# Performance work log

Hardware: AMD Instinct MI355X
Metric: run time of the kernel (lower is better)

The kernel has to match this reference:

```python
import jax, jax.numpy as jnp
import numpy as np

NUM_CLASSES = 10  # matches label fill_max; original iterates over train_label.unique()


def setup_inputs() -> dict:
    key = jax.random.key(0)
    k1, k2, k3 = jax.random.split(key, 3)
    n, m, d = 8192, 50000, 128
    x = jax.random.normal(k1, (n, d), dtype=jnp.float32)
    train_pts = jax.random.normal(k2, (m, d), dtype=jnp.float32)
    train_label = jax.random.randint(k3, (m,), 0, NUM_CLASSES, dtype=jnp.int32)
    return {"x": x, "train_pts": train_pts, "train_label": train_label, "k": 10}


def reference(x, train_pts, train_label, k):
    # Euclidean distance matrix [n, m]; same math as expand/pow/sum without the
    x2 = jnp.sum(x * x, axis=1, keepdims=True)          # [n, 1]
    y2 = jnp.sum(train_pts * train_pts, axis=1)         # [m]
    sq = x2 + y2[None, :] - 2.0 * (x @ train_pts.T)     # [n, m]
    dist = jnp.sqrt(jnp.maximum(sq, 0.0))
    # k smallest distances -> neighbor indices
    _, idx = jax.lax.top_k(-dist, k)                    # [n, k]
    votes = train_label[idx]                            # [n, k]
    # per-class vote counts; original loop: for lab in sorted unique labels,
    # who = count >= best -> ties go to the LARGEST label
    counts = jnp.sum(jax.nn.one_hot(votes, NUM_CLASSES, dtype=jnp.int32), axis=1)  # [n, C]
    winner = (NUM_CLASSES - 1) - jnp.argmax(counts[:, ::-1], axis=1)
    return winner.astype(train_label.dtype)
```

## Files before the change

kernel.cpp:

```cpp
#include <hip/hip_runtime.h>
#include <float.h>
#include <limits.h>

#define N_Q 8192
#define M_PTS 50000
#define DIM 128
#define KNN 10
#define NCLS 10
#define NCHUNK 16
#define TPC 196
#define CPC 8
#define NCAND (NCHUNK*CPC)
#define NSEL 24
#define TPL 4
#define QPB 64
#define SBIAS 256.0f
#define YTHREADS 200000
#define PTHREADS 232768
#define ATHREADS 232944

typedef __attribute__((ext_vector_type(8))) int i32x8;
typedef __attribute__((ext_vector_type(4))) float f32x4;
typedef unsigned int u32;

__device__ __forceinline__ u32 to_e4m3(float f) {
    u32 u = __float_as_uint(f);
    u32 s = (u >> 24) & 0x80u;
    u32 au = u & 0x7FFFFFFFu;
    if (au > 0x43E00000u) au = 0x43E00000u;
    u32 r = au + 0x0007FFFFu + ((au >> 20) & 1u);
    int e = (int)(r >> 23) - 127;
    if (e < -6) return s;
    return s | (u32)((e + 7) << 3) | ((r >> 20) & 7u);
}

__device__ __forceinline__ u32 pack4_e4m3(float4 v, float sc) {
    return to_e4m3(sc * v.x) | (to_e4m3(sc * v.y) << 8) |
           (to_e4m3(sc * v.z) << 16) | (to_e4m3(sc * v.w) << 24);
}

__global__ __launch_bounds__(256) void prep_kernel(
    const float4* __restrict__ x4, const float4* __restrict__ y4,
    u32* __restrict__ xb8, u32* __restrict__ yt8, float* __restrict__ y2) {
    int t = blockIdx.x * 256 + threadIdx.x;
    if (t < YTHREADS) {
        int T = t >> 6, l = t & 63, nr = l & 15, g = l >> 4;
        const float4* src = y4 + ((size_t)(T * 16 + nr) * DIM + g * 32) / 4;
        u32 w[8];
        float ss = 0.f;
        #pragma unroll
        for (int i = 0; i < 8; ++i) {
            float4 v = src[i];
            ss += v.x * v.x + v.y * v.y + v.z * v.z + v.w * v.w;
            w[i] = pack4_e4m3(v, 1.0f);
        }
        uint4* dst = (uint4*)(yt8 + (size_t)T * 512 + l * 8);
        dst[0] = make_uint4(w[0], w[1], w[2], w[3]);
        dst[1] = make_uint4(w[4], w[5], w[6], w[7]);
        ss += __shfl_xor(ss, 16, 64);
        ss += __shfl_xor(ss, 32, 64);
        if (l < 16) y2[T * 16 + l] = ss;
    } else if (t < PTHREADS) {
        int tx = t - YTHREADS, row = tx >> 2, g = tx & 3;
        const float4* src = x4 + ((size_t)row * DIM + g * 32) / 4;
        u32 w[8];
        #pragma unroll
        for (int i = 0; i < 8; ++i) w[i] = pack4_e4m3(src[i], -2.0f);
        uint4* dst = (uint4*)(xb8 + (size_t)row * 32 + g * 8);
        dst[0] = make_uint4(w[0], w[1], w[2], w[3]);
        dst[1] = make_uint4(w[4], w[5], w[6], w[7]);
    } else if (t < ATHREADS) {
        y2[M_PTS + (t - PTHREADS)] = FLT_MAX;
    }
}

__global__ __launch_bounds__(256, 8) void knn_filter(
    const u32* __restrict__ xb8, const u32* __restrict__ yt8,
    const float* __restrict__ y2, u32* __restrict__ ckey) {
    const int lane = threadIdx.x & 63;
    const int wid  = threadIdx.x >> 6;
    const int g    = lane >> 4;
    const int nrow = lane & 15;
    const int chunk = blockIdx.x;
    const int qb    = blockIdx.y;
    const int qw = qb * QPB + wid * 16;

    i32x8 a = *(const i32x8*)(xb8 + (size_t)(qw + nrow) * 32 + g * 8);

    float ts[4][TPL];
    #pragma unroll
    for (int r = 0; r < 4; ++r)
        #pragma unroll
        for (int l = 0; l < TPL; ++l) ts[r][l] = FLT_MAX;

    const u32* ytp = yt8 + (size_t)chunk * TPC * 512 + lane * 8;
    const float* y2p = y2 + chunk * TPC * 16 + nrow;

    for (int t = 0; t < TPC; ++t) {
        i32x8 b = *(const i32x8*)(ytp + (size_t)t * 512);
        float y2n = y2p[t * 16] + SBIAS;
        f32x4 cq = {y2n, y2n, y2n, y2n};
        f32x4 d = __builtin_amdgcn_mfma_scale_f32_16x16x128_f8f6f4(
            a, b, cq, 0, 0, 0, 0x7F7F7F7F, 0, 0x7F7F7F7F);
        u32 rel = (u32)(t * 16) | (u32)nrow;
        #pragma unroll
        for (int i = 0; i < 4; ++i) {
            float key = __uint_as_float((__float_as_uint(d[i]) & 0xFFFFF000u) | rel);
            float o0 = ts[i][0], o1 = ts[i][1], o2 = ts[i][2];
            ts[i][0] = fminf(o0, key);
            ts[i][1] = __builtin_amdgcn_fmed3f(key, o0, o1);
            ts[i][2] = __builtin_amdgcn_fmed3f(key, o1, o2);
            ts[i][3] = __builtin_amdgcn_fmed3f(key, o2, ts[i][3]);
        }
    }

    __shared__ u32 smem[QPB * 65];
    #pragma unroll
    for (int r = 0; r < 4; ++r) {
        int ql = wid * 16 + g * 4 + r;
        #pragma unroll
        for (int l = 0; l < TPL; ++l)
            smem[ql * 65 + nrow * TPL + l] = __float_as_uint(ts[r][l]);
    }
    __syncthreads();
    if (threadIdx.x < QPB) {
        int ql = threadIdx.x;
        float bs[CPC];
        #pragma unroll
        for (int i = 0; i < CPC; ++i) bs[i] = FLT_MAX;
        for (int e = 0; e < 16 * TPL; ++e) {
            float f = __uint_as_float(smem[ql * 65 + e]);
            #pragma unroll
            for (int q2 = 0; q2 < CPC; ++q2) {
                float mn = fminf(bs[q2], f);
                f = fmaxf(bs[q2], f);
                bs[q2] = mn;
            }
        }
        u32* dst = ckey + ((size_t)(qb * QPB + ql) * NCHUNK + chunk) * CPC;
        #pragma unroll
        for (int i = 0; i < CPC; ++i) dst[i] = __float_as_uint(bs[i]);
    }
}

__global__ __launch_bounds__(256) void knn_finalize(
    const u32* __restrict__ ckey, const float* __restrict__ x,
    const float* __restrict__ y, const int* __restrict__ labels,
    int* __restrict__ out) {
    const int lane = threadIdx.x & 63;
    const int wid  = threadIdx.x >> 6;
    const int qbase = blockIdx.x * 8;
    const int ql = wid * 2 + (lane >> 5);
    const int sl = lane & 31;

    __shared__ u32 skey[8][NCAND];
    __shared__ int sidx[8][NSEL];
    __shared__ double sex[8][NSEL];

    for (int i = threadIdx.x; i < 8 * NCAND; i += 256)
        skey[i >> 7][i & 127] = ckey[(size_t)(qbase + (i >> 7)) * NCAND + (i & 127)];
    __syncthreads();

    {
        u32 ke[4];
        int rank[4];
        #pragma unroll
        for (int r0 = 0; r0 < 4; ++r0) {
            ke[r0] = skey[ql][r0 * 32 + sl];
            rank[r0] = 0;
        }
        for (int j = 0; j < NCAND; ++j) {
            u32 kj = skey[ql][j];
            #pragma unroll
            for (int r0 = 0; r0 < 4; ++r0)
                rank[r0] += (kj < ke[r0] || (kj == ke[r0] && j < r0 * 32 + sl)) ? 1 : 0;
        }
        #pragma unroll
        for (int r0 = 0; r0 < 4; ++r0) {
            if (rank[r0] < NSEL) {
                int e = r0 * 32 + sl;
                sidx[ql][rank[r0]] = (e >> 3) * (TPC * 16) + (int)(ke[r0] & 0xFFFu);
            }
        }
    }
    __syncthreads();

    if (sl < NSEL) {
        const int idx = sidx[ql][sl];
        const float4* xr = (const float4*)(x + (size_t)(qbase + ql) * DIM);
        const float4* yr = (const float4*)(y + (size_t)idx * DIM);
        double dy2 = 0.0, dxy = 0.0;
        #pragma unroll 8
        for (int i = 0; i < 32; ++i) {
            float4 yv = yr[i];
            float4 xv = xr[i];
            dy2 = fma((double)yv.x, (double)yv.x, dy2);
            dy2 = fma((double)yv.y, (double)yv.y, dy2);
            dy2 = fma((double)yv.z, (double)yv.z, dy2);
            dy2 = fma((double)yv.w, (double)yv.w, dy2);
            dxy = fma((double)xv.x, (double)yv.x, dxy);
            dxy = fma((double)xv.y, (double)yv.y, dxy);
            dxy = fma((double)xv.z, (double)yv.z, dxy);
            dxy = fma((double)xv.w, (double)yv.w, dxy);
        }
        sex[ql][sl] = dy2 - 2.0 * dxy;
    }
    __syncthreads();

    if (sl == 0) {
        double tsv[KNN]; int ti[KNN];
        #pragma unroll
        for (int i = 0; i < KNN; ++i) { tsv[i] = 1e300; ti[i] = INT_MAX; }
        #pragma unroll
        for (int c = 0; c < NSEL; ++c) {
            double s = sex[ql][c];
            int id = sidx[ql][c];
            #pragma unroll
            for (int pp = 0; pp < KNN; ++pp) {
                bool lt = (s < tsv[pp]) || (s == tsv[pp] && id < ti[pp]);
                double ns = lt ? tsv[pp] : s;  int nid = lt ? ti[pp] : id;
                tsv[pp] = lt ? s : tsv[pp];    ti[pp] = lt ? id : ti[pp];
                s = ns; id = nid;
            }
        }
        int lab[KNN];
        #pragma unroll
        for (int i = 0; i < KNN; ++i) lab[i] = labels[ti[i]];
        int bestc = 0, bestn = -1;
        #pragma unroll
        for (int c = 0; c < NCLS; ++c) {
            int n = 0;
            #pragma unroll
            for (int i = 0; i < KNN; ++i) n += (lab[i] == c) ? 1 : 0;
            if (n >= bestn) { bestn = n; bestc = c; }
        }
        out[qbase + ql] = bestc;
    }
}

extern "C" void kernel_launch(void* const* d_in, const int* in_sizes, int n_in,
                              void* d_out, int out_size, void* d_ws, size_t ws_size,
                              hipStream_t stream) {
    const float* x      = (const float*)d_in[0];
    const float* y      = (const float*)d_in[1];
    const int*   labels = (const int*)d_in[2];

    char* ws = (char*)d_ws;
    size_t off = 0;
    u32* xb8 = (u32*)(ws + off);    off += (size_t)N_Q * DIM;
    u32* yt8 = (u32*)(ws + off);    off += (size_t)NCHUNK * TPC * 2048;
    float* y2 = (float*)(ws + off); off += (size_t)NCHUNK * TPC * 16 * 4;
    u32* ckey = (u32*)(ws + off);   off += (size_t)N_Q * NCAND * 4;
    int* out = (int*)d_out;

    prep_kernel<<<(ATHREADS + 255) / 256, 256, 0, stream>>>(
        (const float4*)x, (const float4*)y, xb8, yt8, y2);
    knn_filter<<<dim3(NCHUNK, N_Q / QPB), 256, 0, stream>>>(xb8, yt8, y2, ckey);
    knn_finalize<<<N_Q / 8, 256, 0, stream>>>(ckey, x, y, labels, out);
}
```

Measured before the change: 259.2 us.

## Transpose MFMA operands so each lane tracks one query, use hardware fp8 convert

Swaps the A/B operands of the scaled fp8 MFMA so that each lane's four outputs belong to a single query across four train points. Each lane now keeps one top-6 list instead of four top-4 lists, and the shared-memory merge shrinks from 64 to 24 candidates per query. The y2 bias is folded into the prep kernel and loaded as a vector, the loop is unrolled by 4, and the software e4m3 conversion is replaced with the hardware cvt_pk_fp8 instruction. The risk is that a per-lane list of 6 drawn from 4 interleaved columns could drop true neighbours in unusual distributions, and the hardware rounding may differ slightly from the previous software conversion.

```diff
diff --git a/kernel.cpp b/kernel.cpp
--- a/kernel.cpp
+++ b/kernel.cpp
@@ -12,7 +12,7 @@
 #define CPC 8
 #define NCAND (NCHUNK*CPC)
 #define NSEL 24
-#define TPL 4
+#define TPL 6
 #define QPB 64
 #define SBIAS 256.0f
 #define YTHREADS 200000
@@ -23,20 +23,11 @@
 typedef __attribute__((ext_vector_type(4))) float f32x4;
 typedef unsigned int u32;
 
-__device__ __forceinline__ u32 to_e4m3(float f) {
-    u32 u = __float_as_uint(f);
-    u32 s = (u >> 24) & 0x80u;
-    u32 au = u & 0x7FFFFFFFu;
-    if (au > 0x43E00000u) au = 0x43E00000u;
-    u32 r = au + 0x0007FFFFu + ((au >> 20) & 1u);
-    int e = (int)(r >> 23) - 127;
-    if (e < -6) return s;
-    return s | (u32)((e + 7) << 3) | ((r >> 20) & 7u);
-}
-
 __device__ __forceinline__ u32 pack4_e4m3(float4 v, float sc) {
-    return to_e4m3(sc * v.x) | (to_e4m3(sc * v.y) << 8) |
-           (to_e4m3(sc * v.z) << 16) | (to_e4m3(sc * v.w) << 24);
+    u32 w = 0;
+    w = __builtin_amdgcn_cvt_pk_fp8_f32(sc * v.x, sc * v.y, w, false);
+    w = __builtin_amdgcn_cvt_pk_fp8_f32(sc * v.z, sc * v.w, w, true);
+    return w;
 }
 
 __global__ __launch_bounds__(256) void prep_kernel(
@@ -59,7 +50,7 @@
         dst[1] = make_uint4(w[4], w[5], w[6], w[7]);
         ss += __shfl_xor(ss, 16, 64);
         ss += __shfl_xor(ss, 32, 64);
-        if (l < 16) y2[T * 16 + l] = ss;
+        if (l < 16) y2[T * 16 + l] = ss + SBIAS;
     } else if (t < PTHREADS) {
         int tx = t - YTHREADS, row = tx >> 2, g = tx & 3;
         const float4* src = x4 + ((size_t)row * DIM + g * 32) / 4;
@@ -85,42 +76,41 @@
     const int qb    = blockIdx.y;
     const int qw = qb * QPB + wid * 16;
 
-    i32x8 a = *(const i32x8*)(xb8 + (size_t)(qw + nrow) * 32 + g * 8);
-
-    float ts[4][TPL];
+    i32x8 bq = *(const i32x8*)(xb8 + (size_t)(qw + nrow) * 32 + g * 8);
+
+    float ts[TPL];
     #pragma unroll
-    for (int r = 0; r < 4; ++r)
-        #pragma unroll
-        for (int l = 0; l < TPL; ++l) ts[r][l] = FLT_MAX;
+    for (int l = 0; l < TPL; ++l) ts[l] = FLT_MAX;
 
     const u32* ytp = yt8 + (size_t)chunk * TPC * 512 + lane * 8;
-    const float* y2p = y2 + chunk * TPC * 16 + nrow;
-
+    const f32x4* y2p = (const f32x4*)(y2 + chunk * TPC * 16 + g * 4);
+
+    #pragma unroll 4
     for (int t = 0; t < TPC; ++t) {
-        i32x8 b = *(const i32x8*)(ytp + (size_t)t * 512);
-        float y2n = y2p[t * 16] + SBIAS;
-        f32x4 cq = {y2n, y2n, y2n, y2n};
+        i32x8 ay = *(const i32x8*)(ytp + (size_t)t * 512);
+        f32x4 cq = y2p[t * 4];
         f32x4 d = __builtin_amdgcn_mfma_scale_f32_16x16x128_f8f6f4(
-            a, b, cq, 0, 0, 0, 0x7F7F7F7F, 0, 0x7F7F7F7F);
-        u32 rel = (u32)(t * 16) | (u32)nrow;
+            ay, bq, cq, 0, 0, 0, 0x7F7F7F7F, 0, 0x7F7F7F7F);
+        u32 relb = (u32)(t * 16) | (u32)(g * 4);
         #pragma unroll
         for (int i = 0; i < 4; ++i) {
-            float key = __uint_as_float((__float_as_uint(d[i]) & 0xFFFFF000u) | rel);
-            float o0 = ts[i][0], o1 = ts[i][1], o2 = ts[i][2];
-            ts[i][0] = fminf(o0, key);
-            ts[i][1] = __builtin_amdgcn_fmed3f(key, o0, o1);
-            ts[i][2] = __builtin_amdgcn_fmed3f(key, o1, o2);
-            ts[i][3] = __builtin_amdgcn_fmed3f(key, o2, ts[i][3]);
-        }
-    }
-
-    __shared__ u32 smem[QPB * 65];
-    #pragma unroll
-    for (int r = 0; r < 4; ++r) {
-        int ql = wid * 16 + g * 4 + r;
+            float key = __uint_as_float((__float_as_uint(d[i]) & 0xFFFFF000u) | (relb + i));
+            float o0 = ts[0], o1 = ts[1], o2 = ts[2], o3 = ts[3], o4 = ts[4];
+            ts[0] = fminf(o0, key);
+            ts[1] = __builtin_amdgcn_fmed3f(key, o0, o1);
+            ts[2] = __builtin_amdgcn_fmed3f(key, o1, o2);
+            ts[3] = __builtin_amdgcn_fmed3f(key, o2, o3);
+            ts[4] = __builtin_amdgcn_fmed3f(key, o3, o4);
+            ts[5] = __builtin_amdgcn_fmed3f(key, o4, ts[5]);
+        }
+    }
+
+    __shared__ u32 smem[QPB * 25];
+    {
+        int ql = wid * 16 + nrow;
         #pragma unroll
         for (int l = 0; l < TPL; ++l)
-            smem[ql * 65 + nrow * TPL + l] = __float_as_uint(ts[r][l]);
+            smem[ql * 25 + g * TPL + l] = __float_as_uint(ts[l]);
     }
     __syncthreads();
     if (threadIdx.x < QPB) {
@@ -128,8 +118,8 @@
         float bs[CPC];
         #pragma unroll
         for (int i = 0; i < CPC; ++i) bs[i] = FLT_MAX;
-        for (int e = 0; e < 16 * TPL; ++e) {
-            float f = __uint_as_float(smem[ql * 65 + e]);
+        for (int e = 0; e < 4 * TPL; ++e) {
+            float f = __uint_as_float(smem[ql * 25 + e]);
             #pragma unroll
             for (int q2 = 0; q2 < CPC; ++q2) {
                 float mn = fminf(bs[q2], f);
```

Measured after the change: 283.7 us. +9.4%, slower.
